# Performance work log

Measured on AMD Instinct MI355X. Metric: run time of the kernel, lower is better.

## Reference

```python
import jax, jax.numpy as jnp
import numpy as np

B, HW, DIM, HEADS, HEAD_DIM, MLP_DIM, WS = 64, 56, 384, 12, 32, 1536, 7
INNER = HEADS * HEAD_DIM
NEG = -1e9


def _masks():
    ws, d = WS, WS // 2
    ul = np.zeros((ws * ws, ws * ws), np.float32)
    ul[-d * ws:, :-d * ws] = NEG
    ul[:-d * ws, -d * ws:] = NEG
    lr = np.zeros((ws, ws, ws, ws), np.float32)
    lr[:, -d:, :, :-d] = NEG
    lr[:, :-d, :, -d:] = NEG
    return jnp.asarray(ul), jnp.asarray(lr.reshape(ws * ws, ws * ws))


def _rel_indices():
    # pairwise relative 2D offsets between the ws*ws positions in a window
    idx = np.stack(np.meshgrid(np.arange(WS), np.arange(WS), indexing='ij'), -1).reshape(-1, 2)
    rel = idx[None, :, :] - idx[:, None, :] + (WS - 1)  # values in [0, 2*WS-2]
    return jnp.asarray(rel)


def _ln(x, g, b):
    m = x.mean(-1, keepdims=True)
    v = x.var(-1, keepdims=True)
    return (x - m) * jax.lax.rsqrt(v + 1e-5) * g + b


def _window_attention(x, w_qkv, pos_emb, w_out, b_out):
    b = x.shape[0]
    disp = WS // 2
    nw = HW // WS  # windows per side
    x = jnp.roll(x, (-disp, -disp), axis=(1, 2))  # cyclic shift
    qkv = x @ w_qkv  # [b, H, W, 3*inner]
    q, k, v = jnp.split(qkv, 3, axis=-1)

    def part(t):  # b (nw w1) (nw w2) (h d) -> b h (nw*nw) (w1*w2) d
        t = t.reshape(b, nw, WS, nw, WS, HEADS, HEAD_DIM)
        return t.transpose(0, 5, 1, 3, 2, 4, 6).reshape(b, HEADS, nw * nw, WS * WS, HEAD_DIM)

    q, k, v = part(q), part(k), part(v)
    dots = jnp.einsum('bhwid,bhwjd->bhwij', q, k) * (HEAD_DIM ** -0.5)
    rel = _rel_indices()
    dots = dots + pos_emb[rel[..., 0], rel[..., 1]]  # relative position bias
    ul, lr = _masks()
    dots = dots.at[:, :, -nw:].add(ul)            # bottom row of windows
    dots = dots.at[:, :, nw - 1::nw].add(lr)      # rightmost column of windows
    attn = jax.nn.softmax(dots, axis=-1)
    out = jnp.einsum('bhwij,bhwjd->bhwid', attn, v)
    # b h (nw nw) (w1 w2) d -> b (nw w1) (nw w2) (h d)
    out = out.reshape(b, HEADS, nw, nw, WS, WS, HEAD_DIM)
    out = out.transpose(0, 2, 4, 3, 5, 1, 6).reshape(b, HW, HW, INNER)
    out = out @ w_out + b_out
    return jnp.roll(out, (disp, disp), axis=(1, 2))  # cyclic back-shift


def swin_block(x, w_qkv, pos_emb, w_out, b_out, ln1_g, ln1_b, ln2_g, ln2_b,
               w_mlp1, b_mlp1, w_mlp2, b_mlp2):
    x = x + _window_attention(_ln(x, ln1_g, ln1_b), w_qkv, pos_emb, w_out, b_out)
    h = _ln(x, ln2_g, ln2_b)
    h = jax.nn.gelu(h @ w_mlp1 + b_mlp1) @ w_mlp2 + b_mlp2
    return x + h


def setup_inputs() -> dict:
    key = jax.random.key(0)
    ks = jax.random.split(key, 8)
    s = lambda fan_in: fan_in ** -0.5
    return {
        'x': jax.random.normal(ks[0], (B, HW, HW, DIM), jnp.float32),
        'w_qkv': jax.random.normal(ks[1], (DIM, 3 * INNER), jnp.float32) * s(DIM),
        'pos_emb': jax.random.normal(ks[2], (2 * WS - 1, 2 * WS - 1), jnp.float32),
        'w_out': jax.random.normal(ks[3], (INNER, DIM), jnp.float32) * s(INNER),
        'b_out': jnp.zeros((DIM,), jnp.float32),
        'ln1_g': jnp.ones((DIM,), jnp.float32),
        'ln1_b': jnp.zeros((DIM,), jnp.float32),
        'ln2_g': jnp.ones((DIM,), jnp.float32),
        'ln2_b': jnp.zeros((DIM,), jnp.float32),
        'w_mlp1': jax.random.normal(ks[4], (DIM, MLP_DIM), jnp.float32) * s(DIM),
        'b_mlp1': jnp.zeros((MLP_DIM,), jnp.float32),
        'w_mlp2': jax.random.normal(ks[5], (MLP_DIM, DIM), jnp.float32) * s(MLP_DIM),
        'b_mlp2': jnp.zeros((DIM,), jnp.float32),
    }


def reference(x, w_qkv, pos_emb, w_out, b_out, ln1_g, ln1_b, ln2_g, ln2_b,
              w_mlp1, b_mlp1, w_mlp2, b_mlp2):
    return swin_block(x, w_qkv, pos_emb, w_out, b_out, ln1_g, ln1_b, ln2_g, ln2_b,
                      w_mlp1, b_mlp1, w_mlp2, b_mlp2)
```

## Files before the change

kernel.cpp:

```cpp
#include <hip/hip_runtime.h>
#include <stdint.h>
#include <stddef.h>


typedef unsigned short u16;
typedef __attribute__((ext_vector_type(8))) short bf16x8;
typedef __attribute__((ext_vector_type(8))) unsigned short u16x8;
typedef __attribute__((ext_vector_type(4))) float f32x4;
typedef __attribute__((ext_vector_type(2))) float f32x2;

#define HW2 3136

__device__ __forceinline__ u16 f2bf(float f) {
    unsigned u = __float_as_uint(f);
    return (u16)((u + 0x7FFFu + ((u >> 16) & 1u)) >> 16);
}

__device__ __forceinline__ float bf2f(u16 u) {
    return __uint_as_float((unsigned)u << 16);
}

__device__ __forceinline__ f32x4 mfma16(bf16x8 a, bf16x8 b, f32x4 c) {
    return __builtin_amdgcn_mfma_f32_16x16x32_bf16(a, b, c, 0, 0, 0);
}

__device__ __forceinline__ void a_copy16(const void* g, void* l) {
    __builtin_amdgcn_global_load_lds((const __attribute__((address_space(1))) void*)g,
                                     (__attribute__((address_space(3))) void*)l, 16, 0, 0);
}

__device__ __forceinline__ f32x2 ld2(const float* p) { return *(const f32x2*)p; }
__device__ __forceinline__ f32x2 ld2(const u16* p) {
    const unsigned u = *(const unsigned*)p;
    f32x2 r;
    r.x = __uint_as_float(u << 16);
    r.y = __uint_as_float(u & 0xffff0000u);
    return r;
}

__device__ __forceinline__ int xcd_swizzle(int bid, int nwg) {
    const int xcd = bid & 7;
    const int i = bid >> 3;
    const int q = nwg >> 3;
    const int r = nwg & 7;
    const int base = (xcd < r) ? xcd * (q + 1) : r * (q + 1) + (xcd - r) * q;
    return base + i;
}

__global__ __launch_bounds__(256) void wtrans(const float* __restrict__ w,
                                              u16* __restrict__ wt, int K, int N) {
    long tid = (long)blockIdx.x * 256 + threadIdx.x;
    if (tid >= (long)K * N) return;
    int n = (int)(tid / K), k = (int)(tid % K);
    wt[tid] = f2bf(w[(long)k * N + n]);
}

__global__ __launch_bounds__(256) void prep_tab(const float* __restrict__ pe,
                                                float* __restrict__ tab) {
    int tid = blockIdx.x * 256 + threadIdx.x;
    if (tid >= 4 * 2401) return;
    int cb = tid / 2401, rem = tid % 2401;
    int i = rem / 49, j = rem % 49;
    int ix = i % 7, jx = j % 7;
    int iy = i / 7, jy = j / 7;
    float v = pe[(jy - iy + 6) * 13 + (jx - ix + 6)];
    if ((cb & 1) && ((i >= 28) != (j >= 28))) v += -1e9f;
    if ((cb & 2) && ((ix >= 4) != (jx >= 4))) v += -1e9f;
    tab[tid] = v;
}

template <int SHIFT, typename TIN>
__global__ __launch_bounds__(256) void ln_kernel(const TIN* __restrict__ in,
                                                 u16* __restrict__ out,
                                                 const float* __restrict__ gw,
                                                 const float* __restrict__ bw) {
    const int lane = threadIdx.x & 63;
    const int wave = threadIdx.x >> 6;
    const long t = (long)blockIdx.x * 4 + wave;
    const TIN* row = in + t * 384;
    f32x2 v0 = ld2(row + lane * 2);
    f32x2 v1 = ld2(row + 128 + lane * 2);
    f32x2 v2 = ld2(row + 256 + lane * 2);
    float s = v0.x + v0.y + v1.x + v1.y + v2.x + v2.y;
    float q = v0.x * v0.x + v0.y * v0.y + v1.x * v1.x + v1.y * v1.y + v2.x * v2.x + v2.y * v2.y;
#pragma unroll
    for (int m = 1; m < 64; m <<= 1) {
        s += __shfl_xor(s, m);
        q += __shfl_xor(q, m);
    }
    const float mean = s * (1.f / 384.f);
    const float rstd = rsqrtf(q * (1.f / 384.f) - mean * mean + 1e-5f);
    long orow = t;
    if (SHIFT) {
        long b = t / HW2;
        int rem = (int)(t % HW2);
        int y = rem / 56 - 3; if (y < 0) y += 56;
        int x = rem % 56 - 3; if (x < 0) x += 56;
        orow = b * HW2 + y * 56 + x;
    }
    u16* po = out + orow * 384;
#pragma unroll
    for (int p = 0; p < 3; p++) {
        f32x2 vv = (p == 0) ? v0 : ((p == 1) ? v1 : v2);
        f32x2 gg = *(const f32x2*)(gw + p * 128 + lane * 2);
        f32x2 bb = *(const f32x2*)(bw + p * 128 + lane * 2);
        float a0 = (vv.x - mean) * rstd * gg.x + bb.x;
        float a1 = (vv.y - mean) * rstd * gg.y + bb.y;
        unsigned pk = (unsigned)f2bf(a0) | ((unsigned)f2bf(a1) << 16);
        *(unsigned*)(po + p * 128 + lane * 2) = pk;
    }
}

template <int EPI>
__global__ __launch_bounds__(256, 4) void gemm_bf16(const u16* __restrict__ A,
                                                    const u16* __restrict__ Bt,
                                                    int N, int K,
                                                    const float* __restrict__ bias,
                                                    const void* residv,
                                                    float* outf, u16* outb) {
    __shared__ u16 Abuf[8192];
    __shared__ u16 Bbuf[8192];
    const int bid = xcd_swizzle(blockIdx.x, gridDim.x);
    const int ntiles = N >> 7;
    const long m0 = (long)(bid / ntiles) << 7;
    const int n0 = (bid % ntiles) << 7;
    const int lane = threadIdx.x & 63;
    const int wave = threadIdx.x >> 6;
    const int wr = (wave >> 1) << 6;
    const int wc = (wave & 1) << 6;
    const int lr = lane & 15;
    const int g  = lane >> 4;

    const u16* aP0; const u16* aP1; const u16* aP2; const u16* aP3;
    const u16* bP0; const u16* bP1; const u16* bP2; const u16* bP3;
    int d0, d1, d2, d3;
    {
#define STAGE_INIT(j, aP, bP, dd)                                          \
        {                                                                  \
            const int o = (((j << 2) + wave) << 10) + lane * 16;           \
            const int row = o >> 7;                                        \
            const int slot = (o >> 4) & 7;                                 \
            const int ce = ((slot ^ (row & 7)) << 3);                      \
            aP = A + (size_t)(m0 + row) * K + ce;                          \
            bP = Bt + (size_t)(n0 + row) * K + ce;                         \
            dd = o >> 1;                                                   \
        }
        STAGE_INIT(0, aP0, bP0, d0)
        STAGE_INIT(1, aP1, bP1, d1)
        STAGE_INIT(2, aP2, bP2, d2)
        STAGE_INIT(3, aP3, bP3, d3)
#undef STAGE_INIT
    }

    f32x4 acc[4][4];
#pragma unroll
    for (int i = 0; i < 4; i++)
#pragma unroll
        for (int j = 0; j < 4; j++) acc[i][j] = (f32x4){0.f, 0.f, 0.f, 0.f};

    for (int k0 = 0; k0 < K; k0 += 64) {
        __syncthreads();
        a_copy16(aP0, Abuf + d0); a_copy16(bP0, Bbuf + d0); aP0 += 64; bP0 += 64;
        a_copy16(aP1, Abuf + d1); a_copy16(bP1, Bbuf + d1); aP1 += 64; bP1 += 64;
        a_copy16(aP2, Abuf + d2); a_copy16(bP2, Bbuf + d2); aP2 += 64; bP2 += 64;
        a_copy16(aP3, Abuf + d3); a_copy16(bP3, Bbuf + d3); aP3 += 64; bP3 += 64;
        __syncthreads();
#pragma unroll
        for (int t = 0; t < 2; t++) {
            bf16x8 bfr[4];
#pragma unroll
            for (int ni = 0; ni < 4; ni++) {
                const int row = wc + ni * 16 + lr;
                const int slot = ((t << 2) + g) ^ (row & 7);
                bfr[ni] = *(const bf16x8*)(Bbuf + row * 64 + slot * 8);
            }
#pragma unroll
            for (int mi = 0; mi < 4; mi++) {
                const int row = wr + mi * 16 + lr;
                const int slot = ((t << 2) + g) ^ (row & 7);
                const bf16x8 af = *(const bf16x8*)(Abuf + row * 64 + slot * 8);
#pragma unroll
                for (int ni = 0; ni < 4; ni++)
                    acc[mi][ni] = mfma16(af, bfr[ni], acc[mi][ni]);
            }
        }
    }

    const float* residf = (const float*)residv;
    const u16*  residb  = (const u16*)residv;
    const int g4 = g << 2;
    float bs[4];
    if (EPI != 0) {
#pragma unroll
        for (int ni = 0; ni < 4; ni++) bs[ni] = bias[n0 + wc + ni * 16 + lr];
    }
#pragma unroll
    for (int mi = 0; mi < 4; mi++) {
#pragma unroll
        for (int r = 0; r < 4; r++) {
            const long m = m0 + wr + mi * 16 + g4 + r;
            long mo = m;
            if (EPI == 1) {
                long b = m / HW2;
                int rem = (int)(m % HW2);
                int y = rem / 56 + 3; if (y >= 56) y -= 56;
                int x = rem % 56 + 3; if (x >= 56) x -= 56;
                mo = b * HW2 + y * 56 + x;
            }
#pragma unroll
            for (int ni = 0; ni < 4; ni++) {
                const float v = acc[mi][ni][r];
                const int n = n0 + wc + ni * 16 + lr;
                if (EPI == 0) {
                    outb[(size_t)m * N + n] = f2bf(v);
                } else if (EPI == 1) {
                    const size_t o = (size_t)mo * 384 + n;
                    outb[o] = f2bf(residf[o] + v + bs[ni]);
                } else if (EPI == 2) {
                    const float gx = v + bs[ni];
                    const float y = 0.7978845608028654f * gx * (1.f + 0.044715f * gx * gx);
                    const float e = __expf(-2.f * y);
                    outb[(size_t)m * N + n] = f2bf(gx * __builtin_amdgcn_rcpf(1.f + e));
                } else {
                    const size_t o = (size_t)m * 384 + n;
                    outf[o] = bf2f(residb[o]) + v + bs[ni];
                }
            }
        }
    }
}

__global__ __launch_bounds__(256) void attn_kernel(const u16* __restrict__ qkv,
                                                   const float* __restrict__ tab,
                                                   u16* __restrict__ outa) {
    __shared__ u16 sVt[4][2304];
    __shared__ u16 sP[4][4608];
    const int lane = threadIdx.x & 63;
    const int wave = threadIdx.x >> 6;
    const int bid = blockIdx.x;
    const int hg = bid % 3;
    const int win = (bid / 3) & 63;
    const int b = bid / 192;
    const int wy = win >> 3, wx = win & 7;
    const int head = hg * 4 + wave;
    const long wbase = (long)b * HW2 + (long)wy * 392 + wx * 7;
    const int c = lane & 15, g = lane >> 4;
    const int kk = g << 3;

    u16* vt = sVt[wave];
    for (int i = lane; i < 2304; i += 64) vt[i] = 0;
    if (lane < 49) {
        const long mr = wbase + (lane / 7) * 56 + (lane % 7);
        const u16* vr = qkv + mr * 1152 + 768 + head * 32;
#pragma unroll
        for (int u = 0; u < 4; u++) {
            u16x8 vv = *(const u16x8*)(vr + u * 8);
#pragma unroll
            for (int e = 0; e < 8; e++) vt[(u * 8 + e) * 72 + lane] = vv[e];
        }
    }

    bf16x8 aq[4], bk[4];
#pragma unroll
    for (int mi = 0; mi < 4; mi++) {
        int t = mi * 16 + c; t = t > 48 ? 48 : t;
        const long mr = wbase + (t / 7) * 56 + (t % 7);
        aq[mi] = *(const bf16x8*)(qkv + mr * 1152 + head * 32 + kk);
    }
#pragma unroll
    for (int ni = 0; ni < 4; ni++) {
        int t = ni * 16 + c; t = t > 48 ? 48 : t;
        const long mr = wbase + (t / 7) * 56 + (t % 7);
        bk[ni] = *(const bf16x8*)(qkv + mr * 1152 + 384 + head * 32 + kk);
    }

    f32x4 sc[4][4];
#pragma unroll
    for (int i = 0; i < 4; i++)
#pragma unroll
        for (int j = 0; j < 4; j++) sc[i][j] = (f32x4){0.f, 0.f, 0.f, 0.f};
    __builtin_amdgcn_s_setprio(1);
#pragma unroll
    for (int mi = 0; mi < 4; mi++)
#pragma unroll
        for (int ni = 0; ni < 4; ni++) sc[mi][ni] = mfma16(aq[mi], bk[ni], sc[mi][ni]);
    __builtin_amdgcn_s_setprio(0);

    const float* tb = tab + (((wy == 7) ? 1 : 0) | ((wx == 7) ? 2 : 0)) * 2401;
#pragma unroll
    for (int mi = 0; mi < 4; mi++) {
#pragma unroll
        for (int r = 0; r < 4; r++) {
            int i = mi * 16 + (g << 2) + r;
            int ic = i > 48 ? 48 : i;
#pragma unroll
            for (int ni = 0; ni < 4; ni++) {
                int j = ni * 16 + c;
                float sv;
                if (j < 49)
                    sv = sc[mi][ni][r] * 0.17677669529663689f + tb[ic * 49 + j];
                else
                    sv = -3.0e38f;
                sc[mi][ni][r] = sv;
            }
        }
    }

    u16* pp = sP[wave];
#pragma unroll
    for (int mi = 0; mi < 4; mi++) {
#pragma unroll
        for (int r = 0; r < 4; r++) {
            float sm = fmaxf(fmaxf(sc[mi][0][r], sc[mi][1][r]),
                             fmaxf(sc[mi][2][r], sc[mi][3][r]));
            sm = fmaxf(sm, __shfl_xor(sm, 1));
            sm = fmaxf(sm, __shfl_xor(sm, 2));
            sm = fmaxf(sm, __shfl_xor(sm, 4));
            sm = fmaxf(sm, __shfl_xor(sm, 8));
            float p0 = __expf(sc[mi][0][r] - sm);
            float p1 = __expf(sc[mi][1][r] - sm);
            float p2 = __expf(sc[mi][2][r] - sm);
            float p3 = __expf(sc[mi][3][r] - sm);
            float ss = p0 + p1 + p2 + p3;
            ss += __shfl_xor(ss, 1);
            ss += __shfl_xor(ss, 2);
            ss += __shfl_xor(ss, 4);
            ss += __shfl_xor(ss, 8);
            const float ri = 1.f / ss;
            const int i = mi * 16 + (g << 2) + r;
            pp[i * 72 + c] = f2bf(p0 * ri);
            pp[i * 72 + 16 + c] = f2bf(p1 * ri);
            pp[i * 72 + 32 + c] = f2bf(p2 * ri);
            pp[i * 72 + 48 + c] = f2bf(p3 * ri);
        }
    }

    f32x4 oc[4][2];
#pragma unroll
    for (int i = 0; i < 4; i++) {
        oc[i][0] = (f32x4){0.f, 0.f, 0.f, 0.f};
        oc[i][1] = (f32x4){0.f, 0.f, 0.f, 0.f};
    }
    __builtin_amdgcn_s_setprio(1);
#pragma unroll
    for (int ks = 0; ks < 2; ks++) {
        bf16x8 bv0 = *(const bf16x8*)(vt + c * 72 + kk + ks * 32);
        bf16x8 bv1 = *(const bf16x8*)(vt + (16 + c) * 72 + kk + ks * 32);
#pragma unroll
        for (int mi = 0; mi < 4; mi++) {
            bf16x8 ap = *(const bf16x8*)(pp + (mi * 16 + c) * 72 + kk + ks * 32);
            oc[mi][0] = mfma16(ap, bv0, oc[mi][0]);
            oc[mi][1] = mfma16(ap, bv1, oc[mi][1]);
        }
    }
    __builtin_amdgcn_s_setprio(0);

#pragma unroll
    for (int mi = 0; mi < 4; mi++) {
#pragma unroll
        for (int r = 0; r < 4; r++) {
            const int i = mi * 16 + (g << 2) + r;
            if (i < 49) {
                const long mr = wbase + (i / 7) * 56 + (i % 7);
                u16* po = outa + mr * 384 + head * 32;
                po[c] = f2bf(oc[mi][0][r]);
                po[16 + c] = f2bf(oc[mi][1][r]);
            }
        }
    }
}

extern "C" void kernel_launch(void* const* d_in, const int* in_sizes, int n_in,
                              void* d_out, int out_size, void* d_ws, size_t ws_size,
                              hipStream_t stream) {
    (void)in_sizes; (void)n_in; (void)out_size;
    const float* x     = (const float*)d_in[0];
    const float* w_qkv = (const float*)d_in[1];
    const float* pos   = (const float*)d_in[2];
    const float* w_out = (const float*)d_in[3];
    const float* b_out = (const float*)d_in[4];
    const float* ln1g  = (const float*)d_in[5];
    const float* ln1b  = (const float*)d_in[6];
    const float* ln2g  = (const float*)d_in[7];
    const float* ln2b  = (const float*)d_in[8];
    const float* w1    = (const float*)d_in[9];
    const float* b1    = (const float*)d_in[10];
    const float* w2    = (const float*)d_in[11];
    const float* b2    = (const float*)d_in[12];
    float* out = (float*)d_out;
    char* ws = (char*)d_ws;

    u16* wqkvT  = (u16*)(ws + 0);
    u16* woutT  = (u16*)(ws + 884736);
    u16* wm1T   = (u16*)(ws + 1179648);
    u16* wm2T   = (u16*)(ws + 2359296);
    float* tab  = (float*)(ws + 3538944);
    const size_t pool0 = 3577856;
    const size_t avail = (ws_size > pool0) ? ws_size - pool0 : 0;

    int CH = 8;
    while (CH > 2 && (size_t)CH * 3136 * 4608ULL > avail) CH >>= 1;
    const int nchunks = 64 / CH;
    const int rows = CH * HW2;
    const int tiles = rows >> 7;
    u16* bufA = (u16*)(ws + pool0);
    u16* bufB = bufA + (size_t)rows * 384;
    u16* bufC = bufB + (size_t)rows * 1152;
    u16* bufD = bufC + (size_t)rows * 384;

    wtrans<<<1728, 256, 0, stream>>>(w_qkv, wqkvT, 384, 1152);
    wtrans<<<576, 256, 0, stream>>>(w_out, woutT, 384, 384);
    wtrans<<<2304, 256, 0, stream>>>(w1, wm1T, 384, 1536);
    wtrans<<<2304, 256, 0, stream>>>(w2, wm2T, 1536, 384);
    prep_tab<<<38, 256, 0, stream>>>(pos, tab);

    for (int c = 0; c < nchunks; ++c) {
        const float* xc = x + (size_t)c * rows * 384;
        float* oc = out + (size_t)c * rows * 384;
        ln_kernel<1, float><<<rows / 4, 256, 0, stream>>>(xc, bufA, ln1g, ln1b);
        gemm_bf16<0><<<tiles * 9, 256, 0, stream>>>(bufA, wqkvT, 1152, 384,
                                                    nullptr, nullptr, nullptr, bufB);
        attn_kernel<<<CH * 192, 256, 0, stream>>>(bufB, tab, bufC);
        gemm_bf16<1><<<tiles * 3, 256, 0, stream>>>(bufC, woutT, 384, 384,
                                                    b_out, xc, nullptr, bufD);
        ln_kernel<0, u16><<<rows / 4, 256, 0, stream>>>(bufD, bufA, ln2g, ln2b);
        gemm_bf16<2><<<tiles * 12, 256, 0, stream>>>(bufA, wm1T, 1536, 384,
                                                     b1, nullptr, nullptr, bufB);
        gemm_bf16<3><<<tiles * 3, 256, 0, stream>>>(bufB, wm2T, 384, 1536,
                                                    b2, bufD, oc, nullptr);
    }
}
```

Baseline: 1.571 ms.

## Process attention P·V per 16-row tile to shrink shared P buffer

Restructures the softmax and P·V stage of the window-attention kernel so each 16-row tile of probabilities is written to a small per-wave LDS buffer, consumed immediately by MFMA, and stored out before the next tile. This cuts the P scratch from 4608 to 1152 elements per wave and drops the 8 live accumulator vectors to 2. The aim is lower LDS and register use so more blocks fit per CU. The cost is that P·V is serialized per tile behind an explicit lgkmcnt wait and sched barriers, which limits overlap inside a wave. It also relies on wave-local LDS ordering, with no barrier between reusing the buffer across tiles.

```diff
diff --git a/kernel.cpp b/kernel.cpp
--- a/kernel.cpp
+++ b/kernel.cpp
@@ -234,7 +234,7 @@
                                                    const float* __restrict__ tab,
                                                    u16* __restrict__ outa) {
     __shared__ u16 sVt[4][2304];
-    __shared__ u16 sP[4][4608];
+    __shared__ u16 sP[4][1152];
     const int lane = threadIdx.x & 63;
     const int wave = threadIdx.x >> 6;
     const int bid = blockIdx.x;
@@ -307,6 +307,7 @@
     }
 
     u16* pp = sP[wave];
+    const int g4 = g << 2;
 #pragma unroll
     for (int mi = 0; mi < 4; mi++) {
 #pragma unroll
@@ -327,44 +328,37 @@
             ss += __shfl_xor(ss, 4);
             ss += __shfl_xor(ss, 8);
             const float ri = 1.f / ss;
-            const int i = mi * 16 + (g << 2) + r;
-            pp[i * 72 + c] = f2bf(p0 * ri);
-            pp[i * 72 + 16 + c] = f2bf(p1 * ri);
-            pp[i * 72 + 32 + c] = f2bf(p2 * ri);
-            pp[i * 72 + 48 + c] = f2bf(p3 * ri);
-        }
-    }
-
-    f32x4 oc[4][2];
-#pragma unroll
-    for (int i = 0; i < 4; i++) {
-        oc[i][0] = (f32x4){0.f, 0.f, 0.f, 0.f};
-        oc[i][1] = (f32x4){0.f, 0.f, 0.f, 0.f};
-    }
-    __builtin_amdgcn_s_setprio(1);
-#pragma unroll
-    for (int ks = 0; ks < 2; ks++) {
-        bf16x8 bv0 = *(const bf16x8*)(vt + c * 72 + kk + ks * 32);
-        bf16x8 bv1 = *(const bf16x8*)(vt + (16 + c) * 72 + kk + ks * 32);
-#pragma unroll
-        for (int mi = 0; mi < 4; mi++) {
-            bf16x8 ap = *(const bf16x8*)(pp + (mi * 16 + c) * 72 + kk + ks * 32);
-            oc[mi][0] = mfma16(ap, bv0, oc[mi][0]);
-            oc[mi][1] = mfma16(ap, bv1, oc[mi][1]);
-        }
-    }
-    __builtin_amdgcn_s_setprio(0);
-
-#pragma unroll
-    for (int mi = 0; mi < 4; mi++) {
+            const int a = g4 + r;
+            pp[a * 72 + c] = f2bf(p0 * ri);
+            pp[a * 72 + 16 + c] = f2bf(p1 * ri);
+            pp[a * 72 + 32 + c] = f2bf(p2 * ri);
+            pp[a * 72 + 48 + c] = f2bf(p3 * ri);
+        }
+        asm volatile("s_waitcnt lgkmcnt(0)" ::: "memory");
+        __builtin_amdgcn_sched_barrier(0);
+
+        f32x4 oc0 = (f32x4){0.f, 0.f, 0.f, 0.f};
+        f32x4 oc1 = (f32x4){0.f, 0.f, 0.f, 0.f};
+        __builtin_amdgcn_s_setprio(1);
+#pragma unroll
+        for (int ks = 0; ks < 2; ks++) {
+            const bf16x8 ap = *(const bf16x8*)(pp + c * 72 + ks * 32 + kk);
+            const bf16x8 bv0 = *(const bf16x8*)(vt + c * 72 + kk + ks * 32);
+            const bf16x8 bv1 = *(const bf16x8*)(vt + (16 + c) * 72 + kk + ks * 32);
+            oc0 = mfma16(ap, bv0, oc0);
+            oc1 = mfma16(ap, bv1, oc1);
+        }
+        __builtin_amdgcn_s_setprio(0);
+        __builtin_amdgcn_sched_barrier(0);
+
 #pragma unroll
         for (int r = 0; r < 4; r++) {
-            const int i = mi * 16 + (g << 2) + r;
+            const int i = mi * 16 + g4 + r;
             if (i < 49) {
                 const long mr = wbase + (i / 7) * 56 + (i % 7);
                 u16* po = outa + mr * 384 + head * 32;
-                po[c] = f2bf(oc[mi][0][r]);
-                po[16 + c] = f2bf(oc[mi][1][r]);
+                po[c] = f2bf(oc0[r]);
+                po[16 + c] = f2bf(oc1[r]);
             }
         }
     }
```

After: 1.578 ms. No clear change (+0.4%).
